# Optimization experiments

Hardware: AMD Instinct MI355X
Metric: run time of the kernel (lower is better)

## Reference

```python
import jax, jax.numpy as jnp
import numpy as np

B, S, E = 2, 2049, 512
H, WIN = 8, 1024
D = E // H


def setup_inputs() -> dict:
    key = jax.random.key(0)
    ks = jax.random.split(key, 11)
    sc = 0.02
    return {
        "x": jax.random.normal(ks[0], (B, S, E), dtype=jnp.float32),
        "Wq": jax.random.normal(ks[1], (E, E), dtype=jnp.float32) * sc,
        "bq": jnp.zeros((E,), dtype=jnp.float32),
        "Wk": jax.random.normal(ks[2], (E, E), dtype=jnp.float32) * sc,
        "bk": jnp.zeros((E,), dtype=jnp.float32),
        "Wv": jax.random.normal(ks[3], (E, E), dtype=jnp.float32) * sc,
        "bv": jnp.zeros((E,), dtype=jnp.float32),
        "Wo": jax.random.normal(ks[4], (E, E), dtype=jnp.float32) * sc,
        "bo": jnp.zeros((E,), dtype=jnp.float32),
        "w_gate": jax.random.normal(ks[5], (2 * E,), dtype=jnp.float32) * sc,
        "b_gate": jnp.zeros((), dtype=jnp.float32),
    }


def reference(x, Wq, bq, Wk, bk, Wv, bv, Wo, bo, w_gate, b_gate):
    scale = D ** -0.5
    q_flat = x @ Wq + bq  # [B,S,E]
    k_flat = x @ Wk + bk
    v_flat = x @ Wv + bv
    q = q_flat.reshape(B, S, H, D).transpose(0, 2, 1, 3)  # [B,H,S,D]
    k = k_flat.reshape(B, S, H, D).transpose(0, 2, 1, 3)
    v = v_flat.reshape(B, S, H, D).transpose(0, 2, 1, 3)

    scores = jnp.einsum("bhqd,bhkd->bhqk", q, k) * scale  # [B,H,S,S]

    # Gaussian positional bias: -0.5*|i-j|^2/sigma^2, sigma = window/2
    pos = jnp.arange(S)
    dist = jnp.abs(pos[:, None] - pos[None, :]).astype(jnp.float32)
    sigma = WIN / 2.0
    bias = -0.5 * dist ** 2 / (sigma ** 2)  # [S,S]
    scores = scores + bias[None, None]

    # Pairwise gate: sigmoid(concat(q_i,k_j) @ w + b) == sigmoid(q_i.wq + k_j.wk + b)
    gq = q_flat @ w_gate[:E]       # [B,S]
    gk = k_flat @ w_gate[E:]       # [B,S]
    gates = jax.nn.sigmoid(gq[:, :, None] + gk[:, None, :] + b_gate)  # [B,S,S]
    scores = scores * gates[:, None]  # broadcast over heads

    local_mask = jnp.where(dist <= WIN, 0.0, -jnp.inf).astype(jnp.float32)
    scores = scores + local_mask[None, None]

    attn = jax.nn.softmax(scores, axis=-1)
    out = jnp.einsum("bhqk,bhkd->bhqd", attn, v)  # [B,H,S,D]
    out = out.transpose(0, 2, 1, 3).reshape(B, S, E)
    return out @ Wo + bo
```

## Files before the change

### kernel.cpp

```cpp
#include <hip/hip_runtime.h>
#include <cstdint>
#include <cstddef>

#define B_ 2
#define S_ 2049
#define E_ 512
#define H_ 8
#define WIN_ 1024
#define MROWS (B_*S_)
#define SP_ 2176
#define GBUFN 4104
#define BHS_ (B_*H_*S_)

typedef unsigned short ushort_t;
typedef __attribute__((ext_vector_type(8))) short bf16x8;
typedef __attribute__((ext_vector_type(4))) float f32x4;

#define MFMA16(a,b,c) __builtin_amdgcn_mfma_f32_16x16x32_bf16(a,b,c,0,0,0)

__device__ __forceinline__ ushort_t f2bf(float f) {
  unsigned int u = __float_as_uint(f);
  u += 0x7fffu + ((u >> 16) & 1u);
  return (ushort_t)(u >> 16);
}
__device__ __forceinline__ float bf2f(ushort_t h) {
  return __uint_as_float(((unsigned int)h) << 16);
}

__global__ __launch_bounds__(256) void convert_all_kernel(
    const float* __restrict__ x, const float* __restrict__ W0,
    const float* __restrict__ W1, const float* __restrict__ W2,
    const float* __restrict__ W3, ushort_t* __restrict__ xb,
    ushort_t* __restrict__ Wt_all, ushort_t* __restrict__ WoHi,
    float* __restrict__ gacc)
{
  __shared__ float tile[32][33];
  int bid = blockIdx.x;
  if (bid < 2049) {
    int idx = bid * 256 + threadIdx.x;
    float4 v = ((const float4*)x)[idx];
    ushort4 o;
    o.x = f2bf(v.x); o.y = f2bf(v.y); o.z = f2bf(v.z); o.w = f2bf(v.w);
    ((ushort4*)xb)[idx] = o;
    return;
  }
  int wid = bid - 2049;
  int z = wid >> 8, rem = wid & 255;
  if (z == 3) {
    int gz = rem * 256 + threadIdx.x;
    if (gz < 2 * GBUFN) gacc[gz] = 0.f;
  }
  const float* W = (z == 0) ? W0 : (z == 1) ? W1 : (z == 2) ? W2 : W3;
  int k0 = (rem >> 4) * 32, n0 = (rem & 15) * 32;
  int r = threadIdx.x >> 5, c = threadIdx.x & 31;
#pragma unroll
  for (int i = 0; i < 4; ++i) {
    int rr = r + i * 8;
    tile[rr][c] = W[(size_t)(k0 + rr) * E_ + n0 + c];
  }
  __syncthreads();
#pragma unroll
  for (int i = 0; i < 4; ++i) {
    int rr = r + i * 8;
    float v = tile[c][rr];
    size_t dst = (size_t)(n0 + rr) * E_ + k0 + c;
    if (z < 3) Wt_all[(size_t)z * E_ * E_ + dst] = f2bf(v);
    else       WoHi[dst] = f2bf(v);
  }
}

__global__ __launch_bounds__(256) void gemm_qkv_kernel(
    const ushort_t* __restrict__ xb, const ushort_t* __restrict__ Wt_all,
    const float* __restrict__ bq, const float* __restrict__ bk,
    const float* __restrict__ bv, const float* __restrict__ wg,
    ushort_t* __restrict__ qkb, ushort_t* __restrict__ vT,
    float* __restrict__ gacc)
{
  __shared__ __align__(16) ushort_t As[64][40];
  __shared__ __align__(16) ushort_t Bs[128][40];
  int tid = threadIdx.x;
  int lane = tid & 63, w = tid >> 6;
  int l15 = lane & 15, quad = lane >> 4;
  int wm = (w & 1) * 32, wn = (w >> 1) * 64;
  int z = blockIdx.z;
  const ushort_t* Wt = Wt_all + (size_t)z * E_ * E_;
  const float* bias = (z == 0) ? bq : (z == 1) ? bk : bv;
  int bt = blockIdx.x;
  int bg2 = bt / 33;
  int bm = (bt - bg2 * 33) * 64;
  int bn = blockIdx.y * 128;
  size_t rowbase = (size_t)bg2 * S_;

  int ar = tid >> 2, acq = (tid & 3) * 8;
  int ai = bm + ar; if (ai >= S_) ai = S_ - 1;
  const ushort_t* ap = xb + (rowbase + ai) * E_ + acq;
  int br = tid >> 1, bcq = (tid & 1) * 16;
  const ushort_t* bp = Wt + (size_t)(bn + br) * E_ + bcq;

  const f32x4 fz = {0.f, 0.f, 0.f, 0.f};
  f32x4 acc[2][4];
#pragma unroll
  for (int mt = 0; mt < 2; ++mt)
#pragma unroll
    for (int nt = 0; nt < 4; ++nt) acc[mt][nt] = fz;

  int4 pa = *(const int4*)ap;
  int4 pb0 = *(const int4*)bp, pb1 = *(const int4*)(bp + 8);

  for (int k0 = 0; k0 < E_; k0 += 32) {
    __syncthreads();
    int kn = (k0 + 32 < E_) ? (k0 + 32) : k0;
    int4 na = *(const int4*)(ap + kn);
    int4 nb0 = *(const int4*)(bp + kn), nb1 = *(const int4*)(bp + kn + 8);
    *(int4*)&As[ar][acq] = pa;
    *(int4*)&Bs[br][bcq] = pb0; *(int4*)&Bs[br][bcq + 8] = pb1;
    __syncthreads();
    bf16x8 a[2], bfr[4];
#pragma unroll
    for (int mt = 0; mt < 2; ++mt) a[mt] = *(const bf16x8*)&As[wm + mt * 16 + l15][quad * 8];
#pragma unroll
    for (int nt = 0; nt < 4; ++nt) bfr[nt] = *(const bf16x8*)&Bs[wn + nt * 16 + l15][quad * 8];
#pragma unroll
    for (int mt = 0; mt < 2; ++mt)
#pragma unroll
      for (int nt = 0; nt < 4; ++nt)
        acc[mt][nt] = MFMA16(a[mt], bfr[nt], acc[mt][nt]);
    pa = na; pb0 = nb0; pb1 = nb1;
  }

  float bb[4];
#pragma unroll
  for (int nt = 0; nt < 4; ++nt) bb[nt] = bias[bn + wn + nt * 16 + l15];

  if (z < 2) {
    ushort_t* C = qkb + (size_t)z * MROWS * E_;
#pragma unroll
    for (int mt = 0; mt < 2; ++mt)
#pragma unroll
      for (int nt = 0; nt < 4; ++nt)
#pragma unroll
        for (int r = 0; r < 4; ++r) {
          int i = bm + wm + mt * 16 + quad * 4 + r;
          if (i < S_)
            C[(rowbase + i) * E_ + bn + wn + nt * 16 + l15] = f2bf(acc[mt][nt][r] + bb[nt]);
        }
    const float* wgp = wg + (size_t)z * E_;
    float wv[4];
#pragma unroll
    for (int nt = 0; nt < 4; ++nt) wv[nt] = wgp[bn + wn + nt * 16 + l15];
    float* gp = gacc + (size_t)z * GBUFN;
#pragma unroll
    for (int mt = 0; mt < 2; ++mt)
#pragma unroll
      for (int r = 0; r < 4; ++r) {
        float s = 0.f;
#pragma unroll
        for (int nt = 0; nt < 4; ++nt) s = fmaf(acc[mt][nt][r] + bb[nt], wv[nt], s);
        s += __shfl_xor(s, 1, 16); s += __shfl_xor(s, 2, 16);
        s += __shfl_xor(s, 4, 16); s += __shfl_xor(s, 8, 16);
        int i = bm + wm + mt * 16 + quad * 4 + r;
        if (l15 == 0 && i < S_) atomicAdd(&gp[rowbase + i], s);
      }
  } else {
    ushort_t* lt = &Bs[0][0];
    int ti = tid >> 2, tc = (tid & 3) * 16;
#pragma unroll
    for (int hh = 0; hh < 2; ++hh) {
      __syncthreads();
      if ((w >> 1) == hh) {
#pragma unroll
        for (int mt = 0; mt < 2; ++mt)
#pragma unroll
          for (int nt = 0; nt < 4; ++nt) {
            int d = nt * 16 + l15;
#pragma unroll
            for (int r = 0; r < 4; ++r) {
              int il = wm + mt * 16 + quad * 4 + r;
              lt[d * 72 + il] = f2bf(acc[mt][nt][r] + bb[nt]);
            }
          }
      }
      __syncthreads();
      int hg = (bn >> 6) + hh;
      union { int4 q[2]; ushort_t u[16]; } tv;
      tv.q[0] = *(const int4*)&lt[ti * 72 + tc];
      tv.q[1] = *(const int4*)&lt[ti * 72 + tc + 8];
      size_t vrow = ((size_t)(bg2 * H_ + hg) * 64 + ti) * SP_;
#pragma unroll
      for (int c8 = 0; c8 < 2; ++c8) {
        int i2 = bm + tc + c8 * 8;
        if (i2 + 7 < S_) {
          *(int4*)&vT[vrow + i2] = tv.q[c8];
        } else {
#pragma unroll
          for (int e = 0; e < 8; ++e)
            if (i2 + e < S_) vT[vrow + i2 + e] = tv.u[c8 * 8 + e];
        }
      }
    }
  }
}

__global__ __launch_bounds__(256) void attn_kernel(
    const ushort_t* __restrict__ qb, const ushort_t* __restrict__ kb,
    const ushort_t* __restrict__ vT, const float* __restrict__ gq_raw,
    const float* __restrict__ gk_raw, const float* __restrict__ bgate,
    float* __restrict__ Opart, float* __restrict__ Lpart)
{
  __shared__ __align__(16) ushort_t Ks[64][72];
  __shared__ __align__(16) ushort_t Vt[64][72];
  __shared__ __align__(16) ushort_t Ps[4][16][72];
  __shared__ float gbs[704];

  int tid = threadIdx.x;
  int lane = tid & 63, w = tid >> 6;
  int l15 = lane & 15, quad = lane >> 4;

  int sub = blockIdx.x % 48;
  int qidx = blockIdx.x / 48;
  int off = (qidx + 1) >> 1;
  int qt = 16 + ((qidx & 1) ? -off : off);
  int bh = sub & 15, third = sub >> 4;
  int h = bh & 7, b = bh >> 3;
  int i0 = qt * 64;
  const float LOG2E = 1.44269504f;
  const float coef2 = (-0.5f / (512.f * 512.f)) * LOG2E;
  const float QSC = 0.125f * LOG2E;

  int i = i0 + w * 16 + l15;
  int ic = (i < S_) ? i : S_ - 1;
  bf16x8 qf0 = *(const bf16x8*)&qb[((size_t)(b * S_ + ic)) * E_ + h * 64 + quad * 8];
  bf16x8 qf1 = *(const bf16x8*)&qb[((size_t)(b * S_ + ic)) * E_ + h * 64 + 32 + quad * 8];
#pragma unroll
  for (int e = 0; e < 8; ++e) {
    qf0[e] = (short)f2bf(bf2f((ushort_t)qf0[e]) * QSC);
    qf1[e] = (short)f2bf(bf2f((ushort_t)qf1[e]) * QSC);
  }
  float av = __expf(-(gq_raw[b * S_ + ic] + bgate[0]));
  float fdi = (i < S_) ? (float)i : -1e5f;

  int jlo = i0 - WIN_; if (jlo < 0) jlo = 0;
  int jt_lo = jlo >> 6;
  int jhi = i0 + 63 + WIN_; if (jhi > S_ - 1) jhi = S_ - 1;
  int jt_hi = jhi >> 6;
  int L = jt_hi - jt_lo + 1;
  int n0 = (L + 2) / 3, n1 = (L + 1) / 3;
  int myLo = jt_lo + ((third == 0) ? 0 : (third == 1) ? n0 : n0 + n1);
  int cnt = (third == 0) ? n0 : (third == 1) ? n1 : L - n0 - n1;
  int myHi = myLo + cnt - 1;
  int jbase = myLo << 6;
  int nwin = cnt << 6;

  for (int tt = tid; tt < nwin; tt += 256) {
    int j = jbase + tt; int jc = (j < S_) ? j : S_ - 1;
    gbs[tt] = __expf(-gk_raw[b * S_ + jc]);
  }

  int srow = tid >> 2, scol = (tid & 3) * 16;
  const ushort_t* kb_base = kb + (size_t)b * S_ * E_ + h * 64 + scol;
  const ushort_t* vb_base = vT + ((size_t)(b * H_ + h) * 64 + srow) * SP_ + scol;

  int4 ka0, ka1, va0, va1;
  {
    int jc0 = jbase + srow; if (jc0 > S_ - 1) jc0 = S_ - 1;
    const int4* kp = (const int4*)(kb_base + (size_t)jc0 * E_);
    ka0 = kp[0]; ka1 = kp[1];
    const int4* vp = (const int4*)(vb_base + jbase);
    va0 = vp[0]; va1 = vp[1];
  }

  const f32x4 fz = {0.f, 0.f, 0.f, 0.f};
  f32x4 Ov[4] = {fz, fz, fz, fz};
  float l_run = 0.f;

  for (int jt = myLo; jt <= myHi; ++jt) {
    int j0 = jt << 6;
    __syncthreads();
    int jn = (jt < myHi) ? ((jt + 1) << 6) : j0;
    int jcn = jn + srow; if (jcn > S_ - 1) jcn = S_ - 1;
    const int4* kp = (const int4*)(kb_base + (size_t)jcn * E_);
    int4 nk0 = kp[0], nk1 = kp[1];
    const int4* vp = (const int4*)(vb_base + jn);
    int4 nv0 = vp[0], nv1 = vp[1];
    *(int4*)&Ks[srow][scol] = ka0; *(int4*)&Ks[srow][scol + 8] = ka1;
    *(int4*)&Vt[srow][scol] = va0; *(int4*)&Vt[srow][scol + 8] = va1;
    __syncthreads();

    f32x4 st[4];
#pragma unroll
    for (int nt = 0; nt < 4; ++nt) {
      bf16x8 kf0 = *(const bf16x8*)&Ks[nt * 16 + l15][quad * 8];
      bf16x8 kf1 = *(const bf16x8*)&Ks[nt * 16 + l15][32 + quad * 8];
      f32x4 s = MFMA16(kf0, qf0, fz);
      st[nt] = MFMA16(kf1, qf1, s);
    }

    bool full = ((j0 + 63 - i0) <= WIN_) && ((i0 + 63 - j0) <= WIN_)
                && (j0 + 63 < S_) && (i0 + 63 < S_);
    float ps = 0.f;
    float fq = fdi - (float)(j0 + quad * 4);
    if (full) {
#pragma unroll
      for (int nt = 0; nt < 4; ++nt) {
        f32x4 g4 = *(const f32x4*)&gbs[(j0 - jbase) + nt * 16 + quad * 4];
#pragma unroll
        for (int r = 0; r < 4; ++r) {
          float f = fq - (float)(nt * 16 + r);
          float gate = __builtin_amdgcn_rcpf(fmaf(av, g4[r], 1.f));
          float p = __builtin_amdgcn_exp2f(fmaf(f * f, coef2, st[nt][r]) * gate);
          st[nt][r] = p; ps += p;
        }
      }
    } else {
#pragma unroll
      for (int nt = 0; nt < 4; ++nt) {
        f32x4 g4 = *(const f32x4*)&gbs[(j0 - jbase) + nt * 16 + quad * 4];
#pragma unroll
        for (int r = 0; r < 4; ++r) {
          int j = j0 + nt * 16 + quad * 4 + r;
          float fj = (j < S_) ? (float)j : 1e5f;
          float f = fdi - fj;
          float gate = __builtin_amdgcn_rcpf(fmaf(av, g4[r], 1.f));
          float t = fmaf(f * f, coef2, st[nt][r]) * gate;
          t = (__builtin_fabsf(f) <= 1024.f) ? t : -1e30f;
          float p = __builtin_amdgcn_exp2f(t);
          st[nt][r] = p; ps += p;
        }
      }
    }
    ps += __shfl_xor(ps, 16);
    ps += __shfl_xor(ps, 32);
    l_run += ps;

#pragma unroll
    for (int nt = 0; nt < 4; ++nt) {
      uint2 pk;
      pk.x = (unsigned int)f2bf(st[nt][0]) | ((unsigned int)f2bf(st[nt][1]) << 16);
      pk.y = (unsigned int)f2bf(st[nt][2]) | ((unsigned int)f2bf(st[nt][3]) << 16);
      *(uint2*)&Ps[w][l15][nt * 16 + quad * 4] = pk;
    }
    bf16x8 p0 = *(const bf16x8*)&Ps[w][l15][quad * 8];
    bf16x8 p1 = *(const bf16x8*)&Ps[w][l15][32 + quad * 8];
#pragma unroll
    for (int nt = 0; nt < 4; ++nt) {
      bf16x8 v0 = *(const bf16x8*)&Vt[nt * 16 + l15][quad * 8];
      bf16x8 v1 = *(const bf16x8*)&Vt[nt * 16 + l15][32 + quad * 8];
      Ov[nt] = MFMA16(p0, v0, Ov[nt]);
      Ov[nt] = MFMA16(p1, v1, Ov[nt]);
    }
    ka0 = nk0; ka1 = nk1; va0 = nv0; va1 = nv1;
  }

  if (lane < 16) {
    int irow = i0 + w * 16 + lane;
    if (irow < S_)
      Lpart[(size_t)third * BHS_ + (size_t)(b * H_ + h) * S_ + irow] = l_run;
  }
#pragma unroll
  for (int r = 0; r < 4; ++r) {
    int irow = i0 + w * 16 + quad * 4 + r;
    if (irow < S_) {
      size_t base = ((size_t)third * BHS_ + (size_t)(b * H_ + h) * S_ + irow) * 64;
#pragma unroll
      for (int nt = 0; nt < 4; ++nt)
        Opart[base + nt * 16 + l15] = Ov[nt][r];
    }
  }
}

__global__ __launch_bounds__(256) void combine_kernel(
    const float* __restrict__ Opart, const float* __restrict__ Lpart,
    ushort_t* __restrict__ ahi, ushort_t* __restrict__ alo)
{
  int tid = threadIdx.x;
  int gi = blockIdx.x * 16 + (tid >> 4);
  int d4 = tid & 15;
  int b = gi / (H_ * S_);
  int rem = gi - b * (H_ * S_);
  int h = rem / S_;
  int i = rem - h * S_;
  size_t p0 = (size_t)(b * H_ + h) * S_ + i;
  float l = Lpart[p0] + Lpart[p0 + (size_t)BHS_] + Lpart[p0 + 2 * (size_t)BHS_];
  float inv = 1.f / l;
  const float* op = Opart + p0 * 64 + d4 * 4;
  float4 o1 = *(const float4*)op;
  float4 o2 = *(const float4*)(op + (size_t)BHS_ * 64);
  float4 o3 = *(const float4*)(op + 2 * (size_t)BHS_ * 64);
  float o[4] = {(o1.x + o2.x + o3.x) * inv, (o1.y + o2.y + o3.y) * inv,
                (o1.z + o2.z + o3.z) * inv, (o1.w + o2.w + o3.w) * inv};
  ushort4 hi, lo;
  hi.x = f2bf(o[0]); lo.x = f2bf(o[0] - bf2f(hi.x));
  hi.y = f2bf(o[1]); lo.y = f2bf(o[1] - bf2f(hi.y));
  hi.z = f2bf(o[2]); lo.z = f2bf(o[2] - bf2f(hi.z));
  hi.w = f2bf(o[3]); lo.w = f2bf(o[3] - bf2f(hi.w));
  size_t oidx = ((size_t)b * S_ + i) * E_ + h * 64 + d4 * 4;
  *(ushort4*)&ahi[oidx] = hi;
  *(ushort4*)&alo[oidx] = lo;
}

__global__ __launch_bounds__(256) void gemm_out_kernel(
    const ushort_t* __restrict__ Ahi, const ushort_t* __restrict__ Alo,
    const ushort_t* __restrict__ Whi, const float* __restrict__ bias,
    float* __restrict__ C)
{
  __shared__ __align__(16) ushort_t AsH[64][40];
  __shared__ __align__(16) ushort_t AsL[64][40];
  __shared__ __align__(16) ushort_t BsW[128][40];
  int tid = threadIdx.x;
  int lane = tid & 63, w = tid >> 6;
  int l15 = lane & 15, quad = lane >> 4;
  int wm = (w & 1) * 32, wn = (w >> 1) * 64;
  int bm = blockIdx.x * 64, bn = blockIdx.y * 128;

  int sr = tid >> 2, sc = (tid & 3) * 8;
  int am = bm + sr; if (am >= MROWS) am = MROWS - 1;
  const ushort_t* ahp = Ahi + (size_t)am * E_ + sc;
  const ushort_t* alp = Alo + (size_t)am * E_ + sc;
  int br = tid >> 1, bc = (tid & 1) * 16;
  const ushort_t* bp = Whi + (size_t)(bn + br) * E_ + bc;

  const f32x4 fz = {0.f, 0.f, 0.f, 0.f};
  f32x4 acc[2][4];
#pragma unroll
  for (int mt = 0; mt < 2; ++mt)
#pragma unroll
    for (int nt = 0; nt < 4; ++nt) acc[mt][nt] = fz;

  int4 ph = *(const int4*)ahp, pl = *(const int4*)alp;
  int4 pb0 = *(const int4*)bp, pb1 = *(const int4*)(bp + 8);

  for (int k0 = 0; k0 < E_; k0 += 32) {
    __syncthreads();
    int kn = (k0 + 32 < E_) ? (k0 + 32) : k0;
    int4 nh = *(const int4*)(ahp + kn);
    int4 nl = *(const int4*)(alp + kn);
    int4 nb0 = *(const int4*)(bp + kn), nb1 = *(const int4*)(bp + kn + 8);
    *(int4*)&AsH[sr][sc] = ph;
    *(int4*)&AsL[sr][sc] = pl;
    *(int4*)&BsW[br][bc] = pb0; *(int4*)&BsW[br][bc + 8] = pb1;
    __syncthreads();
    bf16x8 ah[2], al[2], bw[4];
#pragma unroll
    for (int mt = 0; mt < 2; ++mt) {
      ah[mt] = *(const bf16x8*)&AsH[wm + mt * 16 + l15][quad * 8];
      al[mt] = *(const bf16x8*)&AsL[wm + mt * 16 + l15][quad * 8];
    }
#pragma unroll
    for (int nt = 0; nt < 4; ++nt) bw[nt] = *(const bf16x8*)&BsW[wn + nt * 16 + l15][quad * 8];
#pragma unroll
    for (int mt = 0; mt < 2; ++mt)
#pragma unroll
      for (int nt = 0; nt < 4; ++nt) {
        acc[mt][nt] = MFMA16(ah[mt], bw[nt], acc[mt][nt]);
        acc[mt][nt] = MFMA16(al[mt], bw[nt], acc[mt][nt]);
      }
    ph = nh; pl = nl; pb0 = nb0; pb1 = nb1;
  }
#pragma unroll
  for (int nt = 0; nt < 4; ++nt) {
    float bb = bias[bn + wn + nt * 16 + l15];
#pragma unroll
    for (int mt = 0; mt < 2; ++mt)
#pragma unroll
      for (int r = 0; r < 4; ++r) {
        int m = bm + wm + mt * 16 + quad * 4 + r;
        if (m < MROWS)
          C[(size_t)m * E_ + bn + wn + nt * 16 + l15] = acc[mt][nt][r] + bb;
      }
  }
}

extern "C" void kernel_launch(void* const* d_in, const int* in_sizes, int n_in,
                              void* d_out, int out_size, void* d_ws, size_t ws_size,
                              hipStream_t stream) {
  const float* x  = (const float*)d_in[0];
  const float* Wq = (const float*)d_in[1];
  const float* bq = (const float*)d_in[2];
  const float* Wk = (const float*)d_in[3];
  const float* bk = (const float*)d_in[4];
  const float* Wv = (const float*)d_in[5];
  const float* bv = (const float*)d_in[6];
  const float* Wo = (const float*)d_in[7];
  const float* bo = (const float*)d_in[8];
  const float* wg = (const float*)d_in[9];
  const float* bg = (const float*)d_in[10];

  char* p = (char*)d_ws;
  ushort_t* Wt_all = (ushort_t*)p; p += (size_t)3 * E_ * E_ * 2;
  ushort_t* WoHi   = (ushort_t*)p; p += (size_t)E_ * E_ * 2;
  ushort_t* qkb    = (ushort_t*)p; p += (size_t)2 * MROWS * E_ * 2;
  ushort_t* vT     = (ushort_t*)p; p += (size_t)B_ * H_ * 64 * SP_ * 2;
  float*    gacc   = (float*)p;    p += (size_t)2 * GBUFN * 4;
  float*    Opart  = (float*)p;    p += (size_t)3 * BHS_ * 64 * 4;
  float*    Lpart  = (float*)p;    p += (size_t)3 * BHS_ * 4;
  ushort_t* xb     = (ushort_t*)Opart;
  ushort_t* aHi    = qkb;
  ushort_t* aLo    = qkb + (size_t)MROWS * E_;

  hipLaunchKernelGGL(convert_all_kernel, dim3(3073), dim3(256), 0, stream,
                     x, Wq, Wk, Wv, Wo, xb, Wt_all, WoHi, gacc);
  hipLaunchKernelGGL(gemm_qkv_kernel, dim3(66, 4, 3), dim3(256), 0, stream,
                     xb, Wt_all, bq, bk, bv, wg, qkb, vT, gacc);
  hipLaunchKernelGGL(attn_kernel, dim3(33 * 48), dim3(256), 0, stream,
                     qkb, qkb + (size_t)MROWS * E_, vT, gacc, gacc + GBUFN, bg,
                     Opart, Lpart);
  hipLaunchKernelGGL(combine_kernel, dim3(2049), dim3(256), 0, stream,
                     Opart, Lpart, aHi, aLo);
  hipLaunchKernelGGL(gemm_out_kernel, dim3(65, 4), dim3(256), 0, stream,
                     aHi, aLo, WoHi, bo, (float*)d_out);
}
```

Before: 164.1 us.

## Fuse attention split-K combine into attn kernel via intra-block halves; retile out GEMM

```diff
diff --git a/kernel.cpp b/kernel.cpp
--- a/kernel.cpp
+++ b/kernel.cpp
@@ -10,7 +10,6 @@
 #define MROWS (B_*S_)
 #define SP_ 2176
 #define GBUFN 4104
-#define BHS_ (B_*H_*S_)
 
 typedef unsigned short ushort_t;
 typedef __attribute__((ext_vector_type(8))) short bf16x8;
@@ -201,33 +200,34 @@
   }
 }
 
-__global__ __launch_bounds__(256) void attn_kernel(
+__global__ __launch_bounds__(512) void attn_kernel(
     const ushort_t* __restrict__ qb, const ushort_t* __restrict__ kb,
     const ushort_t* __restrict__ vT, const float* __restrict__ gq_raw,
     const float* __restrict__ gk_raw, const float* __restrict__ bgate,
-    float* __restrict__ Opart, float* __restrict__ Lpart)
+    ushort_t* __restrict__ aHi, ushort_t* __restrict__ aLo)
 {
-  __shared__ __align__(16) ushort_t Ks[64][72];
-  __shared__ __align__(16) ushort_t Vt[64][72];
-  __shared__ __align__(16) ushort_t Ps[4][16][72];
-  __shared__ float gbs[704];
+  __shared__ __align__(16) ushort_t Ks[2][64][72];
+  __shared__ __align__(16) ushort_t Vt[2][64][72];
+  __shared__ __align__(16) ushort_t Ps[8][16][72];
+  __shared__ __align__(16) float gbs[2][1088];
 
   int tid = threadIdx.x;
   int lane = tid & 63, w = tid >> 6;
   int l15 = lane & 15, quad = lane >> 4;
-
-  int sub = blockIdx.x % 48;
-  int qidx = blockIdx.x / 48;
+  int iw = w & 3, jhalf = w >> 2;
+  int t256 = tid & 255;
+
+  int sub = blockIdx.x & 15;
+  int qidx = blockIdx.x >> 4;
   int off = (qidx + 1) >> 1;
   int qt = 16 + ((qidx & 1) ? -off : off);
-  int bh = sub & 15, third = sub >> 4;
-  int h = bh & 7, b = bh >> 3;
+  int h = sub & 7, b = sub >> 3;
   int i0 = qt * 64;
   const float LOG2E = 1.44269504f;
   const float coef2 = (-0.5f / (512.f * 512.f)) * LOG2E;
   const float QSC = 0.125f * LOG2E;
 
-  int i = i0 + w * 16 + l15;
+  int i = i0 + iw * 16 + l15;
   int ic = (i < S_) ? i : S_ - 1;
   bf16x8 qf0 = *(const bf16x8*)&qb[((size_t)(b * S_ + ic)) * E_ + h * 64 + quad * 8];
   bf16x8 qf1 = *(const bf16x8*)&qb[((size_t)(b * S_ + ic)) * E_ + h * 64 + 32 + quad * 8];
@@ -244,19 +244,19 @@
   int jhi = i0 + 63 + WIN_; if (jhi > S_ - 1) jhi = S_ - 1;
   int jt_hi = jhi >> 6;
   int L = jt_hi - jt_lo + 1;
-  int n0 = (L + 2) / 3, n1 = (L + 1) / 3;
-  int myLo = jt_lo + ((third == 0) ? 0 : (third == 1) ? n0 : n0 + n1);
-  int cnt = (third == 0) ? n0 : (third == 1) ? n1 : L - n0 - n1;
-  int myHi = myLo + cnt - 1;
+  int n0 = (L + 1) >> 1, n1 = L - n0;
+  int myLo = jt_lo + (jhalf ? n0 : 0);
+  int cnt = jhalf ? n1 : n0;
+  int cmax = n0;
   int jbase = myLo << 6;
   int nwin = cnt << 6;
 
-  for (int tt = tid; tt < nwin; tt += 256) {
+  for (int tt = t256; tt < nwin; tt += 256) {
     int j = jbase + tt; int jc = (j < S_) ? j : S_ - 1;
-    gbs[tt] = __expf(-gk_raw[b * S_ + jc]);
-  }
-
-  int srow = tid >> 2, scol = (tid & 3) * 16;
+    gbs[jhalf][tt] = __expf(-gk_raw[b * S_ + jc]);
+  }
+
+  int srow = t256 >> 2, scol = (t256 & 3) * 16;
   const ushort_t* kb_base = kb + (size_t)b * S_ * E_ + h * 64 + scol;
   const ushort_t* vb_base = vT + ((size_t)(b * H_ + h) * 64 + srow) * SP_ + scol;
 
@@ -273,129 +273,124 @@
   f32x4 Ov[4] = {fz, fz, fz, fz};
   float l_run = 0.f;
 
-  for (int jt = myLo; jt <= myHi; ++jt) {
-    int j0 = jt << 6;
+  for (int t = 0; t < cmax; ++t) {
+    int act = (t < cnt);
+    int j0 = (myLo + t) << 6;
+    int4 nk0, nk1, nv0, nv1;
     __syncthreads();
-    int jn = (jt < myHi) ? ((jt + 1) << 6) : j0;
-    int jcn = jn + srow; if (jcn > S_ - 1) jcn = S_ - 1;
-    const int4* kp = (const int4*)(kb_base + (size_t)jcn * E_);
-    int4 nk0 = kp[0], nk1 = kp[1];
-    const int4* vp = (const int4*)(vb_base + jn);
-    int4 nv0 = vp[0], nv1 = vp[1];
-    *(int4*)&Ks[srow][scol] = ka0; *(int4*)&Ks[srow][scol + 8] = ka1;
-    *(int4*)&Vt[srow][scol] = va0; *(int4*)&Vt[srow][scol + 8] = va1;
+    if (act) {
+      int jn = (t + 1 < cnt) ? (j0 + 64) : j0;
+      int jcn = jn + srow; if (jcn > S_ - 1) jcn = S_ - 1;
+      const int4* kp = (const int4*)(kb_base + (size_t)jcn * E_);
+      nk0 = kp[0]; nk1 = kp[1];
+      const int4* vp = (const int4*)(vb_base + jn);
+      nv0 = vp[0]; nv1 = vp[1];
+      *(int4*)&Ks[jhalf][srow][scol] = ka0; *(int4*)&Ks[jhalf][srow][scol + 8] = ka1;
+      *(int4*)&Vt[jhalf][srow][scol] = va0; *(int4*)&Vt[jhalf][srow][scol + 8] = va1;
+    }
     __syncthreads();
-
-    f32x4 st[4];
-#pragma unroll
-    for (int nt = 0; nt < 4; ++nt) {
-      bf16x8 kf0 = *(const bf16x8*)&Ks[nt * 16 + l15][quad * 8];
-      bf16x8 kf1 = *(const bf16x8*)&Ks[nt * 16 + l15][32 + quad * 8];
-      f32x4 s = MFMA16(kf0, qf0, fz);
-      st[nt] = MFMA16(kf1, qf1, s);
+    if (act) {
+      f32x4 st[4];
+      __builtin_amdgcn_s_setprio(1);
+#pragma unroll
+      for (int nt = 0; nt < 4; ++nt) {
+        bf16x8 kf0 = *(const bf16x8*)&Ks[jhalf][nt * 16 + l15][quad * 8];
+        bf16x8 kf1 = *(const bf16x8*)&Ks[jhalf][nt * 16 + l15][32 + quad * 8];
+        f32x4 s = MFMA16(kf0, qf0, fz);
+        st[nt] = MFMA16(kf1, qf1, s);
+      }
+      __builtin_amdgcn_s_setprio(0);
+
+      bool full = ((j0 + 63 - i0) <= WIN_) && ((i0 + 63 - j0) <= WIN_)
+                  && (j0 + 63 < S_) && (i0 + 63 < S_);
+      float ps = 0.f;
+      float fq = fdi - (float)(j0 + quad * 4);
+      if (full) {
+#pragma unroll
+        for (int nt = 0; nt < 4; ++nt) {
+          f32x4 g4 = *(const f32x4*)&gbs[jhalf][(j0 - jbase) + nt * 16 + quad * 4];
+#pragma unroll
+          for (int r = 0; r < 4; ++r) {
+            float f = fq - (float)(nt * 16 + r);
+            float gate = __builtin_amdgcn_rcpf(fmaf(av, g4[r], 1.f));
+            float p = __builtin_amdgcn_exp2f(fmaf(f * f, coef2, st[nt][r]) * gate);
+            st[nt][r] = p; ps += p;
+          }
+        }
+      } else {
+#pragma unroll
+        for (int nt = 0; nt < 4; ++nt) {
+          f32x4 g4 = *(const f32x4*)&gbs[jhalf][(j0 - jbase) + nt * 16 + quad * 4];
+#pragma unroll
+          for (int r = 0; r < 4; ++r) {
+            int j = j0 + nt * 16 + quad * 4 + r;
+            float fj = (j < S_) ? (float)j : 1e5f;
+            float f = fdi - fj;
+            float gate = __builtin_amdgcn_rcpf(fmaf(av, g4[r], 1.f));
+            float t2 = fmaf(f * f, coef2, st[nt][r]) * gate;
+            t2 = (__builtin_fabsf(f) <= 1024.f) ? t2 : -1e30f;
+            float p = __builtin_amdgcn_exp2f(t2);
+            st[nt][r] = p; ps += p;
+          }
+        }
+      }
+      ps += __shfl_xor(ps, 16);
+      ps += __shfl_xor(ps, 32);
+      l_run += ps;
+
+#pragma unroll
+      for (int nt = 0; nt < 4; ++nt) {
+        uint2 pk;
+        pk.x = (unsigned int)f2bf(st[nt][0]) | ((unsigned int)f2bf(st[nt][1]) << 16);
+        pk.y = (unsigned int)f2bf(st[nt][2]) | ((unsigned int)f2bf(st[nt][3]) << 16);
+        *(uint2*)&Ps[w][l15][nt * 16 + quad * 4] = pk;
+      }
+      bf16x8 p0 = *(const bf16x8*)&Ps[w][l15][quad * 8];
+      bf16x8 p1 = *(const bf16x8*)&Ps[w][l15][32 + quad * 8];
+      __builtin_amdgcn_s_setprio(1);
+#pragma unroll
+      for (int nt = 0; nt < 4; ++nt) {
+        bf16x8 v0 = *(const bf16x8*)&Vt[jhalf][nt * 16 + l15][quad * 8];
+        bf16x8 v1 = *(const bf16x8*)&Vt[jhalf][nt * 16 + l15][32 + quad * 8];
+        Ov[nt] = MFMA16(p0, v0, Ov[nt]);
+        Ov[nt] = MFMA16(p1, v1, Ov[nt]);
+      }
+      __builtin_amdgcn_s_setprio(0);
+      ka0 = nk0; ka1 = nk1; va0 = nv0; va1 = nv1;
     }
-
-    bool full = ((j0 + 63 - i0) <= WIN_) && ((i0 + 63 - j0) <= WIN_)
-                && (j0 + 63 < S_) && (i0 + 63 < S_);
-    float ps = 0.f;
-    float fq = fdi - (float)(j0 + quad * 4);
-    if (full) {
-#pragma unroll
-      for (int nt = 0; nt < 4; ++nt) {
-        f32x4 g4 = *(const f32x4*)&gbs[(j0 - jbase) + nt * 16 + quad * 4];
-#pragma unroll
-        for (int r = 0; r < 4; ++r) {
-          float f = fq - (float)(nt * 16 + r);
-          float gate = __builtin_amdgcn_rcpf(fmaf(av, g4[r], 1.f));
-          float p = __builtin_amdgcn_exp2f(fmaf(f * f, coef2, st[nt][r]) * gate);
-          st[nt][r] = p; ps += p;
+  }
+
+  __syncthreads();
+  float* Of = (float*)&Vt[0][0][0];
+  float* Lf = Of + 4096;
+  if (jhalf) {
+#pragma unroll
+    for (int nt = 0; nt < 4; ++nt)
+#pragma unroll
+      for (int r = 0; r < 4; ++r)
+        Of[(iw * 16 + quad * 4 + r) * 64 + nt * 16 + l15] = Ov[nt][r];
+  }
+  if (lane < 16) Lf[jhalf * 64 + iw * 16 + lane] = l_run;
+  __syncthreads();
+  if (!jhalf) {
+#pragma unroll
+    for (int r = 0; r < 4; ++r) {
+      int row = quad * 4 + r;
+      int irow = i0 + iw * 16 + row;
+      if (irow < S_) {
+        float lt = Lf[iw * 16 + row] + Lf[64 + iw * 16 + row];
+        float inv = 1.f / lt;
+#pragma unroll
+        for (int nt = 0; nt < 4; ++nt) {
+          float o = (Ov[nt][r] + Of[(iw * 16 + row) * 64 + nt * 16 + l15]) * inv;
+          ushort_t hi = f2bf(o);
+          ushort_t lo = f2bf(o - bf2f(hi));
+          size_t oidx = ((size_t)b * S_ + irow) * E_ + h * 64 + nt * 16 + l15;
+          aHi[oidx] = hi; aLo[oidx] = lo;
         }
       }
-    } else {
-#pragma unroll
-      for (int nt = 0; nt < 4; ++nt) {
-        f32x4 g4 = *(const f32x4*)&gbs[(j0 - jbase) + nt * 16 + quad * 4];
-#pragma unroll
-        for (int r = 0; r < 4; ++r) {
-          int j = j0 + nt * 16 + quad * 4 + r;
-          float fj = (j < S_) ? (float)j : 1e5f;
-          float f = fdi - fj;
-          float gate = __builtin_amdgcn_rcpf(fmaf(av, g4[r], 1.f));
-          float t = fmaf(f * f, coef2, st[nt][r]) * gate;
-          t = (__builtin_fabsf(f) <= 1024.f) ? t : -1e30f;
-          float p = __builtin_amdgcn_exp2f(t);
-          st[nt][r] = p; ps += p;
-        }
-      }
     }
-    ps += __shfl_xor(ps, 16);
-    ps += __shfl_xor(ps, 32);
-    l_run += ps;
-
-#pragma unroll
-    for (int nt = 0; nt < 4; ++nt) {
-      uint2 pk;
-      pk.x = (unsigned int)f2bf(st[nt][0]) | ((unsigned int)f2bf(st[nt][1]) << 16);
-      pk.y = (unsigned int)f2bf(st[nt][2]) | ((unsigned int)f2bf(st[nt][3]) << 16);
-      *(uint2*)&Ps[w][l15][nt * 16 + quad * 4] = pk;
-    }
-    bf16x8 p0 = *(const bf16x8*)&Ps[w][l15][quad * 8];
-    bf16x8 p1 = *(const bf16x8*)&Ps[w][l15][32 + quad * 8];
-#pragma unroll
-    for (int nt = 0; nt < 4; ++nt) {
-      bf16x8 v0 = *(const bf16x8*)&Vt[nt * 16 + l15][quad * 8];
-      bf16x8 v1 = *(const bf16x8*)&Vt[nt * 16 + l15][32 + quad * 8];
-      Ov[nt] = MFMA16(p0, v0, Ov[nt]);
-      Ov[nt] = MFMA16(p1, v1, Ov[nt]);
-    }
-    ka0 = nk0; ka1 = nk1; va0 = nv0; va1 = nv1;
-  }
-
-  if (lane < 16) {
-    int irow = i0 + w * 16 + lane;
-    if (irow < S_)
-      Lpart[(size_t)third * BHS_ + (size_t)(b * H_ + h) * S_ + irow] = l_run;
-  }
-#pragma unroll
-  for (int r = 0; r < 4; ++r) {
-    int irow = i0 + w * 16 + quad * 4 + r;
-    if (irow < S_) {
-      size_t base = ((size_t)third * BHS_ + (size_t)(b * H_ + h) * S_ + irow) * 64;
-#pragma unroll
-      for (int nt = 0; nt < 4; ++nt)
-        Opart[base + nt * 16 + l15] = Ov[nt][r];
-    }
-  }
-}
-
-__global__ __launch_bounds__(256) void combine_kernel(
-    const float* __restrict__ Opart, const float* __restrict__ Lpart,
-    ushort_t* __restrict__ ahi, ushort_t* __restrict__ alo)
-{
-  int tid = threadIdx.x;
-  int gi = blockIdx.x * 16 + (tid >> 4);
-  int d4 = tid & 15;
-  int b = gi / (H_ * S_);
-  int rem = gi - b * (H_ * S_);
-  int h = rem / S_;
-  int i = rem - h * S_;
-  size_t p0 = (size_t)(b * H_ + h) * S_ + i;
-  float l = Lpart[p0] + Lpart[p0 + (size_t)BHS_] + Lpart[p0 + 2 * (size_t)BHS_];
-  float inv = 1.f / l;
-  const float* op = Opart + p0 * 64 + d4 * 4;
-  float4 o1 = *(const float4*)op;
-  float4 o2 = *(const float4*)(op + (size_t)BHS_ * 64);
-  float4 o3 = *(const float4*)(op + 2 * (size_t)BHS_ * 64);
-  float o[4] = {(o1.x + o2.x + o3.x) * inv, (o1.y + o2.y + o3.y) * inv,
-                (o1.z + o2.z + o3.z) * inv, (o1.w + o2.w + o3.w) * inv};
-  ushort4 hi, lo;
-  hi.x = f2bf(o[0]); lo.x = f2bf(o[0] - bf2f(hi.x));
-  hi.y = f2bf(o[1]); lo.y = f2bf(o[1] - bf2f(hi.y));
-  hi.z = f2bf(o[2]); lo.z = f2bf(o[2] - bf2f(hi.z));
-  hi.w = f2bf(o[3]); lo.w = f2bf(o[3] - bf2f(hi.w));
-  size_t oidx = ((size_t)b * S_ + i) * E_ + h * 64 + d4 * 4;
-  *(ushort4*)&ahi[oidx] = hi;
-  *(ushort4*)&alo[oidx] = lo;
+  }
 }
 
 __global__ __launch_bounds__(256) void gemm_out_kernel(
@@ -405,59 +400,58 @@
 {
   __shared__ __align__(16) ushort_t AsH[64][40];
   __shared__ __align__(16) ushort_t AsL[64][40];
-  __shared__ __align__(16) ushort_t BsW[128][40];
+  __shared__ __align__(16) ushort_t BsW[64][40];
   int tid = threadIdx.x;
   int lane = tid & 63, w = tid >> 6;
   int l15 = lane & 15, quad = lane >> 4;
-  int wm = (w & 1) * 32, wn = (w >> 1) * 64;
-  int bm = blockIdx.x * 64, bn = blockIdx.y * 128;
+  int wm = (w & 1) * 32, wn = (w >> 1) * 32;
+  int bm = blockIdx.x * 64, bn = blockIdx.y * 64;
 
   int sr = tid >> 2, sc = (tid & 3) * 8;
   int am = bm + sr; if (am >= MROWS) am = MROWS - 1;
   const ushort_t* ahp = Ahi + (size_t)am * E_ + sc;
   const ushort_t* alp = Alo + (size_t)am * E_ + sc;
-  int br = tid >> 1, bc = (tid & 1) * 16;
-  const ushort_t* bp = Whi + (size_t)(bn + br) * E_ + bc;
+  const ushort_t* bp = Whi + (size_t)(bn + sr) * E_ + sc;
 
   const f32x4 fz = {0.f, 0.f, 0.f, 0.f};
-  f32x4 acc[2][4];
+  f32x4 acc[2][2];
 #pragma unroll
   for (int mt = 0; mt < 2; ++mt)
 #pragma unroll
-    for (int nt = 0; nt < 4; ++nt) acc[mt][nt] = fz;
+    for (int nt = 0; nt < 2; ++nt) acc[mt][nt] = fz;
 
   int4 ph = *(const int4*)ahp, pl = *(const int4*)alp;
-  int4 pb0 = *(const int4*)bp, pb1 = *(const int4*)(bp + 8);
+  int4 pb = *(const int4*)bp;
 
   for (int k0 = 0; k0 < E_; k0 += 32) {
     __syncthreads();
     int kn = (k0 + 32 < E_) ? (k0 + 32) : k0;
     int4 nh = *(const int4*)(ahp + kn);
     int4 nl = *(const int4*)(alp + kn);
-    int4 nb0 = *(const int4*)(bp + kn), nb1 = *(const int4*)(bp + kn + 8);
+    int4 nb = *(const int4*)(bp + kn);
     *(int4*)&AsH[sr][sc] = ph;
     *(int4*)&AsL[sr][sc] = pl;
-    *(int4*)&BsW[br][bc] = pb0; *(int4*)&BsW[br][bc + 8] = pb1;
+    *(int4*)&BsW[sr][sc] = pb;
     __syncthreads();
-    bf16x8 ah[2], al[2], bw[4];
+    bf16x8 ah[2], al[2], bw[2];
 #pragma unroll
     for (int mt = 0; mt < 2; ++mt) {
       ah[mt] = *(const bf16x8*)&AsH[wm + mt * 16 + l15][quad * 8];
       al[mt] = *(const bf16x8*)&AsL[wm + mt * 16 + l15][quad * 8];
     }
 #pragma unroll
-    for (int nt = 0; nt < 4; ++nt) bw[nt] = *(const bf16x8*)&BsW[wn + nt * 16 + l15][quad * 8];
+    for (int nt = 0; nt < 2; ++nt) bw[nt] = *(const bf16x8*)&BsW[wn + nt * 16 + l15][quad * 8];
 #pragma unroll
     for (int mt = 0; mt < 2; ++mt)
 #pragma unroll
-      for (int nt = 0; nt < 4; ++nt) {
+      for (int nt = 0; nt < 2; ++nt) {
         acc[mt][nt] = MFMA16(ah[mt], bw[nt], acc[mt][nt]);
         acc[mt][nt] = MFMA16(al[mt], bw[nt], acc[mt][nt]);
       }
-    ph = nh; pl = nl; pb0 = nb0; pb1 = nb1;
-  }
-#pragma unroll
-  for (int nt = 0; nt < 4; ++nt) {
+    ph = nh; pl = nl; pb = nb;
+  }
+#pragma unroll
+  for (int nt = 0; nt < 2; ++nt) {
     float bb = bias[bn + wn + nt * 16 + l15];
 #pragma unroll
     for (int mt = 0; mt < 2; ++mt)
@@ -491,21 +485,17 @@
   ushort_t* qkb    = (ushort_t*)p; p += (size_t)2 * MROWS * E_ * 2;
   ushort_t* vT     = (ushort_t*)p; p += (size_t)B_ * H_ * 64 * SP_ * 2;
   float*    gacc   = (float*)p;    p += (size_t)2 * GBUFN * 4;
-  float*    Opart  = (float*)p;    p += (size_t)3 * BHS_ * 64 * 4;
-  float*    Lpart  = (float*)p;    p += (size_t)3 * BHS_ * 4;
-  ushort_t* xb     = (ushort_t*)Opart;
-  ushort_t* aHi    = qkb;
-  ushort_t* aLo    = qkb + (size_t)MROWS * E_;
+  ushort_t* xb     = (ushort_t*)p; p += (size_t)MROWS * E_ * 2;
+  ushort_t* aHi    = (ushort_t*)p; p += (size_t)MROWS * E_ * 2;
+  ushort_t* aLo    = (ushort_t*)p; p += (size_t)MROWS * E_ * 2;
 
   hipLaunchKernelGGL(convert_all_kernel, dim3(3073), dim3(256), 0, stream,
                      x, Wq, Wk, Wv, Wo, xb, Wt_all, WoHi, gacc);
   hipLaunchKernelGGL(gemm_qkv_kernel, dim3(66, 4, 3), dim3(256), 0, stream,
                      xb, Wt_all, bq, bk, bv, wg, qkb, vT, gacc);
-  hipLaunchKernelGGL(attn_kernel, dim3(33 * 48), dim3(256), 0, stream,
+  hipLaunchKernelGGL(attn_kernel, dim3(33 * 16), dim3(512), 0, stream,
                      qkb, qkb + (size_t)MROWS * E_, vT, gacc, gacc + GBUFN, bg,
-                     Opart, Lpart);
-  hipLaunchKernelGGL(combine_kernel, dim3(2049), dim3(256), 0, stream,
-                     Opart, Lpart, aHi, aLo);
-  hipLaunchKernelGGL(gemm_out_kernel, dim3(65, 4), dim3(256), 0, stream,
+                     aHi, aLo);
+  hipLaunchKernelGGL(gemm_out_kernel, dim3(65, 8), dim3(256), 0, stream,
                      aHi, aLo, WoHi, bo, (float*)d_out);
 }
```

After: 169.5 us. 3.3% more time.

## Replace split-K partial buffers and combine kernel with atomic accumulation fused into out-projection

Applied to the files above, without the earlier changes.

```diff
diff --git a/kernel.cpp b/kernel.cpp
--- a/kernel.cpp
+++ b/kernel.cpp
@@ -32,7 +32,8 @@
     const float* __restrict__ W1, const float* __restrict__ W2,
     const float* __restrict__ W3, ushort_t* __restrict__ xb,
     ushort_t* __restrict__ Wt_all, ushort_t* __restrict__ WoHi,
-    float* __restrict__ gacc)
+    float* __restrict__ gacc, float* __restrict__ Oacc,
+    float* __restrict__ Lacc)
 {
   __shared__ float tile[32][33];
   int bid = blockIdx.x;
@@ -42,6 +43,8 @@
     ushort4 o;
     o.x = f2bf(v.x); o.y = f2bf(v.y); o.z = f2bf(v.z); o.w = f2bf(v.w);
     ((ushort4*)xb)[idx] = o;
+    float4 z4 = {0.f, 0.f, 0.f, 0.f};
+    ((float4*)Oacc)[idx] = z4;
     return;
   }
   int wid = bid - 2049;
@@ -49,6 +52,7 @@
   if (z == 3) {
     int gz = rem * 256 + threadIdx.x;
     if (gz < 2 * GBUFN) gacc[gz] = 0.f;
+    if (gz < BHS_) Lacc[gz] = 0.f;
   }
   const float* W = (z == 0) ? W0 : (z == 1) ? W1 : (z == 2) ? W2 : W3;
   int k0 = (rem >> 4) * 32, n0 = (rem & 15) * 32;
@@ -205,7 +209,7 @@
     const ushort_t* __restrict__ qb, const ushort_t* __restrict__ kb,
     const ushort_t* __restrict__ vT, const float* __restrict__ gq_raw,
     const float* __restrict__ gk_raw, const float* __restrict__ bgate,
-    float* __restrict__ Opart, float* __restrict__ Lpart)
+    float* __restrict__ Oacc, float* __restrict__ Lacc)
 {
   __shared__ __align__(16) ushort_t Ks[64][72];
   __shared__ __align__(16) ushort_t Vt[64][72];
@@ -287,6 +291,7 @@
     __syncthreads();
 
     f32x4 st[4];
+    __builtin_amdgcn_s_setprio(1);
 #pragma unroll
     for (int nt = 0; nt < 4; ++nt) {
       bf16x8 kf0 = *(const bf16x8*)&Ks[nt * 16 + l15][quad * 8];
@@ -294,6 +299,7 @@
       f32x4 s = MFMA16(kf0, qf0, fz);
       st[nt] = MFMA16(kf1, qf1, s);
     }
+    __builtin_amdgcn_s_setprio(0);
 
     bool full = ((j0 + 63 - i0) <= WIN_) && ((i0 + 63 - j0) <= WIN_)
                 && (j0 + 63 < S_) && (i0 + 63 < S_);
@@ -341,6 +347,7 @@
     }
     bf16x8 p0 = *(const bf16x8*)&Ps[w][l15][quad * 8];
     bf16x8 p1 = *(const bf16x8*)&Ps[w][l15][32 + quad * 8];
+    __builtin_amdgcn_s_setprio(1);
 #pragma unroll
     for (int nt = 0; nt < 4; ++nt) {
       bf16x8 v0 = *(const bf16x8*)&Vt[nt * 16 + l15][quad * 8];
@@ -348,58 +355,29 @@
       Ov[nt] = MFMA16(p0, v0, Ov[nt]);
       Ov[nt] = MFMA16(p1, v1, Ov[nt]);
     }
+    __builtin_amdgcn_s_setprio(0);
     ka0 = nk0; ka1 = nk1; va0 = nv0; va1 = nv1;
   }
 
   if (lane < 16) {
     int irow = i0 + w * 16 + lane;
     if (irow < S_)
-      Lpart[(size_t)third * BHS_ + (size_t)(b * H_ + h) * S_ + irow] = l_run;
+      atomicAdd(&Lacc[(size_t)(b * H_ + h) * S_ + irow], l_run);
   }
 #pragma unroll
   for (int r = 0; r < 4; ++r) {
     int irow = i0 + w * 16 + quad * 4 + r;
     if (irow < S_) {
-      size_t base = ((size_t)third * BHS_ + (size_t)(b * H_ + h) * S_ + irow) * 64;
+      float* op = &Oacc[((size_t)(b * H_ + h) * S_ + irow) * 64];
 #pragma unroll
       for (int nt = 0; nt < 4; ++nt)
-        Opart[base + nt * 16 + l15] = Ov[nt][r];
-    }
-  }
-}
-
-__global__ __launch_bounds__(256) void combine_kernel(
-    const float* __restrict__ Opart, const float* __restrict__ Lpart,
-    ushort_t* __restrict__ ahi, ushort_t* __restrict__ alo)
-{
-  int tid = threadIdx.x;
-  int gi = blockIdx.x * 16 + (tid >> 4);
-  int d4 = tid & 15;
-  int b = gi / (H_ * S_);
-  int rem = gi - b * (H_ * S_);
-  int h = rem / S_;
-  int i = rem - h * S_;
-  size_t p0 = (size_t)(b * H_ + h) * S_ + i;
-  float l = Lpart[p0] + Lpart[p0 + (size_t)BHS_] + Lpart[p0 + 2 * (size_t)BHS_];
-  float inv = 1.f / l;
-  const float* op = Opart + p0 * 64 + d4 * 4;
-  float4 o1 = *(const float4*)op;
-  float4 o2 = *(const float4*)(op + (size_t)BHS_ * 64);
-  float4 o3 = *(const float4*)(op + 2 * (size_t)BHS_ * 64);
-  float o[4] = {(o1.x + o2.x + o3.x) * inv, (o1.y + o2.y + o3.y) * inv,
-                (o1.z + o2.z + o3.z) * inv, (o1.w + o2.w + o3.w) * inv};
-  ushort4 hi, lo;
-  hi.x = f2bf(o[0]); lo.x = f2bf(o[0] - bf2f(hi.x));
-  hi.y = f2bf(o[1]); lo.y = f2bf(o[1] - bf2f(hi.y));
-  hi.z = f2bf(o[2]); lo.z = f2bf(o[2] - bf2f(hi.z));
-  hi.w = f2bf(o[3]); lo.w = f2bf(o[3] - bf2f(hi.w));
-  size_t oidx = ((size_t)b * S_ + i) * E_ + h * 64 + d4 * 4;
-  *(ushort4*)&ahi[oidx] = hi;
-  *(ushort4*)&alo[oidx] = lo;
+        atomicAdd(&op[nt * 16 + l15], Ov[nt][r]);
+    }
+  }
 }
 
 __global__ __launch_bounds__(256) void gemm_out_kernel(
-    const ushort_t* __restrict__ Ahi, const ushort_t* __restrict__ Alo,
+    const float* __restrict__ Oacc, const float* __restrict__ Lacc,
     const ushort_t* __restrict__ Whi, const float* __restrict__ bias,
     float* __restrict__ C)
 {
@@ -414,8 +392,9 @@
 
   int sr = tid >> 2, sc = (tid & 3) * 8;
   int am = bm + sr; if (am >= MROWS) am = MROWS - 1;
-  const ushort_t* ahp = Ahi + (size_t)am * E_ + sc;
-  const ushort_t* alp = Alo + (size_t)am * E_ + sc;
+  int ab = (am >= S_) ? 1 : 0;
+  int ai = am - ab * S_;
+  size_t obase = (size_t)(ab * H_) * S_;
   int br = tid >> 1, bc = (tid & 1) * 16;
   const ushort_t* bp = Whi + (size_t)(bn + br) * E_ + bc;
 
@@ -426,17 +405,41 @@
 #pragma unroll
     for (int nt = 0; nt < 4; ++nt) acc[mt][nt] = fz;
 
-  int4 ph = *(const int4*)ahp, pl = *(const int4*)alp;
+  float4 pa0, pa1; float plv;
+  {
+    int k = sc;
+    int hh = k >> 6, dd = k & 63;
+    const float* oa = Oacc + (obase + (size_t)hh * S_ + ai) * 64 + dd;
+    pa0 = *(const float4*)oa; pa1 = *(const float4*)(oa + 4);
+    plv = Lacc[obase + (size_t)hh * S_ + ai];
+  }
   int4 pb0 = *(const int4*)bp, pb1 = *(const int4*)(bp + 8);
 
   for (int k0 = 0; k0 < E_; k0 += 32) {
     __syncthreads();
     int kn = (k0 + 32 < E_) ? (k0 + 32) : k0;
-    int4 nh = *(const int4*)(ahp + kn);
-    int4 nl = *(const int4*)(alp + kn);
+    float4 na0, na1; float nlv;
+    {
+      int k = kn + sc;
+      int hh = k >> 6, dd = k & 63;
+      const float* oa = Oacc + (obase + (size_t)hh * S_ + ai) * 64 + dd;
+      na0 = *(const float4*)oa; na1 = *(const float4*)(oa + 4);
+      nlv = Lacc[obase + (size_t)hh * S_ + ai];
+    }
     int4 nb0 = *(const int4*)(bp + kn), nb1 = *(const int4*)(bp + kn + 8);
-    *(int4*)&AsH[sr][sc] = ph;
-    *(int4*)&AsL[sr][sc] = pl;
+
+    float inv = 1.f / plv;
+    float oe[8] = {pa0.x, pa0.y, pa0.z, pa0.w, pa1.x, pa1.y, pa1.z, pa1.w};
+    union { int4 q; ushort_t u[8]; } uh, ul;
+#pragma unroll
+    for (int e = 0; e < 8; ++e) {
+      float o = oe[e] * inv;
+      ushort_t hi = f2bf(o);
+      uh.u[e] = hi;
+      ul.u[e] = f2bf(o - bf2f(hi));
+    }
+    *(int4*)&AsH[sr][sc] = uh.q;
+    *(int4*)&AsL[sr][sc] = ul.q;
     *(int4*)&BsW[br][bc] = pb0; *(int4*)&BsW[br][bc + 8] = pb1;
     __syncthreads();
     bf16x8 ah[2], al[2], bw[4];
@@ -454,7 +457,7 @@
         acc[mt][nt] = MFMA16(ah[mt], bw[nt], acc[mt][nt]);
         acc[mt][nt] = MFMA16(al[mt], bw[nt], acc[mt][nt]);
       }
-    ph = nh; pl = nl; pb0 = nb0; pb1 = nb1;
+    pa0 = na0; pa1 = na1; plv = nlv; pb0 = nb0; pb1 = nb1;
   }
 #pragma unroll
   for (int nt = 0; nt < 4; ++nt) {
@@ -491,21 +494,17 @@
   ushort_t* qkb    = (ushort_t*)p; p += (size_t)2 * MROWS * E_ * 2;
   ushort_t* vT     = (ushort_t*)p; p += (size_t)B_ * H_ * 64 * SP_ * 2;
   float*    gacc   = (float*)p;    p += (size_t)2 * GBUFN * 4;
-  float*    Opart  = (float*)p;    p += (size_t)3 * BHS_ * 64 * 4;
-  float*    Lpart  = (float*)p;    p += (size_t)3 * BHS_ * 4;
-  ushort_t* xb     = (ushort_t*)Opart;
-  ushort_t* aHi    = qkb;
-  ushort_t* aLo    = qkb + (size_t)MROWS * E_;
+  ushort_t* xb     = (ushort_t*)p; p += (size_t)MROWS * E_ * 2;
+  float*    Oacc   = (float*)p;    p += (size_t)BHS_ * 64 * 4;
+  float*    Lacc   = (float*)p;    p += (size_t)BHS_ * 4;
 
   hipLaunchKernelGGL(convert_all_kernel, dim3(3073), dim3(256), 0, stream,
-                     x, Wq, Wk, Wv, Wo, xb, Wt_all, WoHi, gacc);
+                     x, Wq, Wk, Wv, Wo, xb, Wt_all, WoHi, gacc, Oacc, Lacc);
   hipLaunchKernelGGL(gemm_qkv_kernel, dim3(66, 4, 3), dim3(256), 0, stream,
                      xb, Wt_all, bq, bk, bv, wg, qkb, vT, gacc);
   hipLaunchKernelGGL(attn_kernel, dim3(33 * 48), dim3(256), 0, stream,
                      qkb, qkb + (size_t)MROWS * E_, vT, gacc, gacc + GBUFN, bg,
-                     Opart, Lpart);
-  hipLaunchKernelGGL(combine_kernel, dim3(2049), dim3(256), 0, stream,
-                     Opart, Lpart, aHi, aLo);
+                     Oacc, Lacc);
   hipLaunchKernelGGL(gemm_out_kernel, dim3(65, 4), dim3(256), 0, stream,
-                     aHi, aLo, WoHi, bo, (float*)d_out);
-}
+                     Oacc, Lacc, WoHi, bo, (float*)d_out);
+}
```

New measurement: 167.0 us. Within noise of the previous version (+1.8%).
